# Optimization experiments

Hardware: AMD Instinct MI355X
Metric: run time of the kernel (lower is better)

## Reference

```python
import jax, jax.numpy as jnp
import numpy as np

B, N, D = 2, 2048, 1024
H, DH = 16, 64
INNER = H * DH  # 1024
EPS = 1e-5


def setup_inputs() -> dict:
    key = jax.random.key(0)
    ks = jax.random.split(key, 7)
    x = jax.random.normal(ks[0], (B, N, D), dtype=jnp.float32)
    mask = jax.random.uniform(ks[1], (B, N)) < 0.9
    mask = mask.at[:, 0].set(True)  # guarantee at least one valid key per row
    attn_bias = jax.random.normal(ks[2], (H, N, N), dtype=jnp.float32) * 0.02
    ln_w = jnp.ones((D,), dtype=jnp.float32)
    ln_b = jnp.zeros((D,), dtype=jnp.float32)
    wq = jax.random.normal(ks[3], (D, INNER), dtype=jnp.float32) * 0.02
    wkv = jax.random.normal(ks[4], (D, 2 * DH), dtype=jnp.float32) * 0.02
    wo = jax.random.normal(ks[5], (INNER, D), dtype=jnp.float32) * 0.02
    return {"x": x, "attn_bias": attn_bias, "ln_w": ln_w, "ln_b": ln_b,
            "wq": wq, "wkv": wkv, "wo": wo, "mask": mask}


def reference(x, attn_bias, ln_w, ln_b, wq, wkv, wo, mask):
    scale = DH ** -0.5
    # NOTE: in the torch module, kv_input = x BEFORE self.norm (context=None),
    # so K/V come from raw x while Q comes from LayerNorm(x).
    mu = jnp.mean(x, axis=-1, keepdims=True)
    var = jnp.var(x, axis=-1, keepdims=True)
    xn = (x - mu) / jnp.sqrt(var + EPS) * ln_w + ln_b
    q = (xn @ wq).reshape(B, N, H, DH).transpose(0, 2, 1, 3) * scale  # b h n d
    kv = x @ wkv                     # b n 2*dh (shared single KV head, MQA)
    k, v = kv[..., :DH], kv[..., DH:]
    sim = jnp.einsum('bhid,bjd->bhij', q, k) + attn_bias  # bias broadcasts over b
    mask_value = -jnp.finfo(sim.dtype).max
    sim = jnp.where(mask[:, None, None, :], sim, mask_value)
    attn = jax.nn.softmax(sim, axis=-1)
    out = jnp.einsum('bhij,bjd->bhid', attn, v)
    out = out.transpose(0, 2, 1, 3).reshape(B, N, INNER)
    return out @ wo
```

## Files before the change

### kernel.cpp

```cpp
#include <hip/hip_runtime.h>
#include <hip/hip_bf16.h>

typedef __bf16 bf16_t;
typedef __bf16 bf16x4 __attribute__((ext_vector_type(4)));
typedef __bf16 bf16x8 __attribute__((ext_vector_type(8)));
typedef float f32x4 __attribute__((ext_vector_type(4)));

static constexpr int BB    = 2;
static constexpr int SEQ   = 2048;
static constexpr int DM    = 1024;
static constexpr int NHEAD = 16;
static constexpr int HD    = 64;
static constexpr float L2E = 1.4426950408889634f;

__device__ __forceinline__ bf16x8 ld8(const bf16_t* p) {
  return *reinterpret_cast<const bf16x8*>(p);
}

__device__ __forceinline__ void gl_lds16(const bf16_t* g, bf16_t* l) {
  __builtin_amdgcn_global_load_lds(
      (const __attribute__((address_space(1))) void*)g,
      (__attribute__((address_space(3))) void*)l, 16, 0, 0);
}

__device__ __forceinline__ uint2 shfl2(uint2 v, int src) {
  uint2 r;
  r.x = (unsigned)__shfl((int)v.x, src, 64);
  r.y = (unsigned)__shfl((int)v.y, src, 64);
  return r;
}

template <typename T> __device__ __forceinline__ T cvt_out(float v);
template <> __device__ __forceinline__ float  cvt_out<float >(float v) { return v; }
template <> __device__ __forceinline__ bf16_t cvt_out<bf16_t>(float v) { return (bf16_t)v; }

__global__ __launch_bounds__(256) void transpose_cast(const float* __restrict__ in,
                                                      bf16_t* __restrict__ out,
                                                      int R, int C) {
  __shared__ float tile[32][33];
  const int c0 = blockIdx.x * 32, r0 = blockIdx.y * 32;
  const int tx = threadIdx.x & 31, ty = threadIdx.x >> 5;
#pragma unroll
  for (int y = ty; y < 32; y += 8)
    tile[y][tx] = in[(size_t)(r0 + y) * C + (c0 + tx)];
  __syncthreads();
#pragma unroll
  for (int y = ty; y < 32; y += 8)
    out[(size_t)(c0 + y) * R + (r0 + tx)] = (bf16_t)tile[tx][y];
}

__global__ __launch_bounds__(256) void row_prep(const float* __restrict__ x,
    const float* __restrict__ ln_w, const float* __restrict__ ln_b,
    const int* __restrict__ mask,
    bf16_t* __restrict__ xbf, bf16_t* __restrict__ xn, float* __restrict__ maskA) {
  const int row = blockIdx.x, t = threadIdx.x;
  __shared__ float red[8];
  const float4 xv = *reinterpret_cast<const float4*>(&x[(size_t)row * DM + t * 4]);
  float s  = xv.x + xv.y + xv.z + xv.w;
  float s2 = xv.x * xv.x + xv.y * xv.y + xv.z * xv.z + xv.w * xv.w;
#pragma unroll
  for (int off = 32; off >= 1; off >>= 1) {
    s  += __shfl_xor(s,  off, 64);
    s2 += __shfl_xor(s2, off, 64);
  }
  if ((t & 63) == 0) { red[t >> 6] = s; red[4 + (t >> 6)] = s2; }
  __syncthreads();
  s  = red[0] + red[1] + red[2] + red[3];
  s2 = red[4] + red[5] + red[6] + red[7];
  const float mu   = s * (1.0f / DM);
  const float var  = s2 * (1.0f / DM) - mu * mu;
  const float rstd = rsqrtf(var + 1e-5f);
  const float4 wv = *reinterpret_cast<const float4*>(&ln_w[t * 4]);
  const float4 bv = *reinterpret_cast<const float4*>(&ln_b[t * 4]);
  union { bf16_t h[4]; uint2 u; } p0, p1;
  p0.h[0] = (bf16_t)xv.x; p0.h[1] = (bf16_t)xv.y;
  p0.h[2] = (bf16_t)xv.z; p0.h[3] = (bf16_t)xv.w;
  p1.h[0] = (bf16_t)((xv.x - mu) * rstd * wv.x + bv.x);
  p1.h[1] = (bf16_t)((xv.y - mu) * rstd * wv.y + bv.y);
  p1.h[2] = (bf16_t)((xv.z - mu) * rstd * wv.z + bv.z);
  p1.h[3] = (bf16_t)((xv.w - mu) * rstd * wv.w + bv.w);
  *reinterpret_cast<uint2*>(&xbf[(size_t)row * DM + t * 4]) = p0.u;
  *reinterpret_cast<uint2*>(&xn [(size_t)row * DM + t * 4]) = p1.u;
  if (t == 0) maskA[row] = mask[row] ? 0.0f : -1e30f;
}

template <typename OutT>
__global__ __launch_bounds__(256) void gemm128(const bf16_t* __restrict__ A,
    const bf16_t* __restrict__ Bt, OutT* __restrict__ C,
    int M, int Nn, int K, float scale) {
  __shared__ alignas(16) bf16_t As[128 * 32];
  __shared__ alignas(16) bf16_t Bs[128 * 32];
  const int m0 = blockIdx.x * 128, n0 = blockIdx.y * 128;
  const int t = threadIdx.x, lane = t & 63, w = t >> 6;
  const int wm = (w & 1) * 64, wn = (w >> 1) * 64;
  const int l15 = lane & 15, q4 = lane >> 4;
  f32x4 acc[4][4] = {};
  const int sr = lane >> 2, sc = (lane & 3) * 8;
  const bf16_t* Ap0 = A  + (size_t)(m0 + w * 32 + sr) * K + sc;
  const bf16_t* Ap1 = Ap0 + (size_t)16 * K;
  const bf16_t* Bp0 = Bt + (size_t)(n0 + w * 32 + sr) * K + sc;
  const bf16_t* Bp1 = Bp0 + (size_t)16 * K;
  bf16_t* AsL0 = &As[(w * 32) * 32];
  bf16_t* AsL1 = &As[(w * 32 + 16) * 32];
  bf16_t* BsL0 = &Bs[(w * 32) * 32];
  bf16_t* BsL1 = &Bs[(w * 32 + 16) * 32];
  for (int k0 = 0; k0 < K; k0 += 32) {
    gl_lds16(Ap0 + k0, AsL0);
    gl_lds16(Ap1 + k0, AsL1);
    gl_lds16(Bp0 + k0, BsL0);
    gl_lds16(Bp1 + k0, BsL1);
    __syncthreads();
    bf16x8 af[4], bfr[4];
#pragma unroll
    for (int mt = 0; mt < 4; ++mt) af[mt]  = ld8(&As[(wm + mt * 16 + l15) * 32 + q4 * 8]);
#pragma unroll
    for (int nt = 0; nt < 4; ++nt) bfr[nt] = ld8(&Bs[(wn + nt * 16 + l15) * 32 + q4 * 8]);
#pragma unroll
    for (int mt = 0; mt < 4; ++mt)
#pragma unroll
      for (int nt = 0; nt < 4; ++nt)
        acc[mt][nt] = __builtin_amdgcn_mfma_f32_16x16x32_bf16(af[mt], bfr[nt], acc[mt][nt], 0, 0, 0);
    __syncthreads();
  }
#pragma unroll
  for (int mt = 0; mt < 4; ++mt)
#pragma unroll
    for (int nt = 0; nt < 4; ++nt)
#pragma unroll
      for (int r = 0; r < 4; ++r) {
        const int gm = m0 + wm + mt * 16 + q4 * 4 + r;
        const int gn = n0 + wn + nt * 16 + l15;
        C[(size_t)gm * Nn + gn] = cvt_out<OutT>(acc[mt][nt][r] * scale);
      }
}

__global__ __launch_bounds__(256) void gemm_kv(const bf16_t* __restrict__ A,
    const bf16_t* __restrict__ Bt, bf16_t* __restrict__ C, bf16_t* __restrict__ C2,
    int M, int Nn, int K) {
  __shared__ alignas(16) bf16_t As[128 * 32];
  __shared__ alignas(16) bf16_t Bs[64 * 32];
  const int m0 = blockIdx.x * 128, n0 = blockIdx.y * 64;
  const int t = threadIdx.x, lane = t & 63, w = t >> 6;
  const int wm = (w & 1) * 64, wn = (w >> 1) * 32;
  const int l15 = lane & 15, q4 = lane >> 4;
  f32x4 acc[4][2] = {};
  const int sr = lane >> 2, sc = (lane & 3) * 8;
  const bf16_t* Ap0 = A  + (size_t)(m0 + w * 32 + sr) * K + sc;
  const bf16_t* Ap1 = Ap0 + (size_t)16 * K;
  const bf16_t* Bp  = Bt + (size_t)(n0 + w * 16 + sr) * K + sc;
  bf16_t* AsL0 = &As[(w * 32) * 32];
  bf16_t* AsL1 = &As[(w * 32 + 16) * 32];
  bf16_t* BsL  = &Bs[(w * 16) * 32];
  for (int k0 = 0; k0 < K; k0 += 32) {
    gl_lds16(Ap0 + k0, AsL0);
    gl_lds16(Ap1 + k0, AsL1);
    gl_lds16(Bp  + k0, BsL);
    __syncthreads();
    bf16x8 af[4], bfr[2];
#pragma unroll
    for (int mt = 0; mt < 4; ++mt) af[mt]  = ld8(&As[(wm + mt * 16 + l15) * 32 + q4 * 8]);
#pragma unroll
    for (int nt = 0; nt < 2; ++nt) bfr[nt] = ld8(&Bs[(wn + nt * 16 + l15) * 32 + q4 * 8]);
#pragma unroll
    for (int mt = 0; mt < 4; ++mt)
#pragma unroll
      for (int nt = 0; nt < 2; ++nt)
        acc[mt][nt] = __builtin_amdgcn_mfma_f32_16x16x32_bf16(af[mt], bfr[nt], acc[mt][nt], 0, 0, 0);
    __syncthreads();
  }
#pragma unroll
  for (int mt = 0; mt < 4; ++mt)
#pragma unroll
    for (int nt = 0; nt < 2; ++nt)
#pragma unroll
      for (int r = 0; r < 4; ++r) {
        const int gm = m0 + wm + mt * 16 + q4 * 4 + r;
        const int gn = n0 + wn + nt * 16 + l15;
        const bf16_t ov = (bf16_t)acc[mt][nt][r];
        if (gn < HD) C[(size_t)gm * HD + gn] = ov;
        else C2[((size_t)(gm >> 11) * HD + (gn - HD)) * SEQ + (gm & 2047)] = ov;
      }
}

__global__ __launch_bounds__(256, 4) void flash_attn(
    const bf16_t* __restrict__ q,
    const bf16_t* __restrict__ kk,
    const bf16_t* __restrict__ vT,
    const float*  __restrict__ bias,
    const float*  __restrict__ maskA,
    bf16_t* __restrict__ aout)
{
  const int b = blockIdx.y & 1, h = blockIdx.y >> 1;
  const int i0 = blockIdx.x * 64;
  const int t = threadIdx.x, lane = t & 63, w = t >> 6;
  const int l15 = lane & 15, q4 = lane >> 4;

  __shared__ alignas(16) bf16_t Ks[2][64][72];
  __shared__ alignas(16) bf16_t Vs[2][64][72];

  const bf16_t* qrow = &q[((size_t)b * SEQ + i0 + w * 16 + l15) * DM + h * HD];
  const bf16x8 bq0 = ld8(qrow + q4 * 8);
  const bf16x8 bq1 = ld8(qrow + 32 + q4 * 8);

  f32x4 o[4] = {};
  float m_run = -1e30f, l_run = 0.0f;

  const float* bias_p = bias + (size_t)h * SEQ * SEQ
                      + (size_t)(i0 + w * 16 + l15) * SEQ + q4 * 4;
  const float* mask_p = maskA + b * SEQ + q4 * 4;

  const int sr = t >> 2, sc = (t & 3) * 16;
  const bf16_t* kp = &kk[((size_t)b * SEQ + sr) * HD + sc];
  const bf16_t* vp = &vT[((size_t)b * HD + sr) * SEQ + sc];

  uint4 kr0 = *reinterpret_cast<const uint4*>(kp);
  uint4 kr1 = *reinterpret_cast<const uint4*>(kp + 8);
  uint4 vr0 = *reinterpret_cast<const uint4*>(vp);
  uint4 vr1 = *reinterpret_cast<const uint4*>(vp + 8);
  f32x4 bv[4], mv[4];
#pragma unroll
  for (int mt = 0; mt < 4; ++mt) {
    bv[mt] = *reinterpret_cast<const f32x4*>(bias_p + mt * 16);
    mv[mt] = *reinterpret_cast<const f32x4*>(mask_p + mt * 16);
  }
  *reinterpret_cast<uint4*>(&Ks[0][sr][sc])     = kr0;
  *reinterpret_cast<uint4*>(&Ks[0][sr][sc + 8]) = kr1;
  *reinterpret_cast<uint4*>(&Vs[0][sr][sc])     = vr0;
  *reinterpret_cast<uint4*>(&Vs[0][sr][sc + 8]) = vr1;
  __syncthreads();

  for (int it = 0; it < SEQ / 64; ++it) {
    const int buf = it & 1;
    const int j1 = (it + 1) * 64;
    const bool more = (j1 < SEQ);
    if (more) {
      kr0 = *reinterpret_cast<const uint4*>(kp + (size_t)j1 * HD);
      kr1 = *reinterpret_cast<const uint4*>(kp + (size_t)j1 * HD + 8);
      vr0 = *reinterpret_cast<const uint4*>(vp + j1);
      vr1 = *reinterpret_cast<const uint4*>(vp + j1 + 8);
    }

    f32x4 s[4];
#pragma unroll
    for (int mt = 0; mt < 4; ++mt) {
      const bf16x8 a0 = ld8(&Ks[buf][mt * 16 + l15][q4 * 8]);
      const bf16x8 a1 = ld8(&Ks[buf][mt * 16 + l15][32 + q4 * 8]);
      f32x4 z = {0.f, 0.f, 0.f, 0.f};
      z = __builtin_amdgcn_mfma_f32_16x16x32_bf16(a0, bq0, z, 0, 0, 0);
      z = __builtin_amdgcn_mfma_f32_16x16x32_bf16(a1, bq1, z, 0, 0, 0);
      s[mt] = z;
    }

    float mx = -1e30f;
#pragma unroll
    for (int mt = 0; mt < 4; ++mt)
#pragma unroll
      for (int r = 0; r < 4; ++r) {
        s[mt][r] = s[mt][r] + bv[mt][r] + mv[mt][r];
        mx = fmaxf(mx, s[mt][r]);
      }
    if (more) {
#pragma unroll
      for (int mt = 0; mt < 4; ++mt) {
        bv[mt] = *reinterpret_cast<const f32x4*>(bias_p + j1 + mt * 16);
        mv[mt] = *reinterpret_cast<const f32x4*>(mask_p + j1 + mt * 16);
      }
    }
    mx = fmaxf(mx, __shfl_xor(mx, 16, 64));
    mx = fmaxf(mx, __shfl_xor(mx, 32, 64));
    const float mnew  = fmaxf(m_run, mx);
    const float alpha = __builtin_amdgcn_exp2f((m_run - mnew) * L2E);
    const float cc    = -mnew * L2E;
    m_run = mnew;

    float su = 0.0f;
#pragma unroll
    for (int mt = 0; mt < 4; ++mt)
#pragma unroll
      for (int r = 0; r < 4; ++r) {
        s[mt][r] = __builtin_amdgcn_exp2f(__builtin_fmaf(s[mt][r], L2E, cc));
        su += s[mt][r];
      }
    su += __shfl_xor(su, 16, 64);
    su += __shfl_xor(su, 32, 64);
    l_run = l_run * alpha + su;

#pragma unroll
    for (int r = 0; r < 4; ++r) {
      const float a_r = __shfl(alpha, q4 * 4 + r, 64);
      o[0][r] *= a_r; o[1][r] *= a_r; o[2][r] *= a_r; o[3][r] *= a_r;
    }

    uint2 pk[4];
#pragma unroll
    for (int mt = 0; mt < 4; ++mt) {
      union { bf16_t hh[4]; uint2 u; } pu;
      pu.hh[0] = (bf16_t)s[mt][0]; pu.hh[1] = (bf16_t)s[mt][1];
      pu.hh[2] = (bf16_t)s[mt][2]; pu.hh[3] = (bf16_t)s[mt][3];
      pk[mt] = pu.u;
    }
    const int src0 = ((q4 & 1) << 5) + l15;
    const int src1 = src0 + 16;
    const bool hiSel = (q4 >> 1) != 0;
#pragma unroll
    for (int ks = 0; ks < 2; ++ks) {
      const uint2 a0 = shfl2(pk[2 * ks],     src0);
      const uint2 a1 = shfl2(pk[2 * ks + 1], src0);
      const uint2 b0 = shfl2(pk[2 * ks],     src1);
      const uint2 b1 = shfl2(pk[2 * ks + 1], src1);
      union { unsigned u[4]; bf16x8 v; } pf;
      pf.u[0] = hiSel ? a1.x : a0.x; pf.u[1] = hiSel ? a1.y : a0.y;
      pf.u[2] = hiSel ? b1.x : b0.x; pf.u[3] = hiSel ? b1.y : b0.y;
#pragma unroll
      for (int nt = 0; nt < 4; ++nt) {
        const bf16x8 vv = ld8(&Vs[buf][nt * 16 + l15][ks * 32 + q4 * 8]);
        o[nt] = __builtin_amdgcn_mfma_f32_16x16x32_bf16(pf.v, vv, o[nt], 0, 0, 0);
      }
    }

    if (more) {
      *reinterpret_cast<uint4*>(&Ks[buf ^ 1][sr][sc])     = kr0;
      *reinterpret_cast<uint4*>(&Ks[buf ^ 1][sr][sc + 8]) = kr1;
      *reinterpret_cast<uint4*>(&Vs[buf ^ 1][sr][sc])     = vr0;
      *reinterpret_cast<uint4*>(&Vs[buf ^ 1][sr][sc + 8]) = vr1;
    }
    __syncthreads();
  }

#pragma unroll
  for (int r = 0; r < 4; ++r) {
    const float linv = 1.0f / __shfl(l_run, q4 * 4 + r, 64);
    const int gi = i0 + w * 16 + q4 * 4 + r;
    bf16_t* dst = &aout[((size_t)b * SEQ + gi) * DM + h * HD];
#pragma unroll
    for (int nt = 0; nt < 4; ++nt)
      dst[nt * 16 + l15] = (bf16_t)(o[nt][r] * linv);
  }
}

extern "C" void kernel_launch(void* const* d_in, const int* in_sizes, int n_in,
                              void* d_out, int out_size, void* d_ws, size_t ws_size,
                              hipStream_t stream) {
  const float* x         = (const float*)d_in[0];
  const float* attn_bias = (const float*)d_in[1];
  const float* ln_w      = (const float*)d_in[2];
  const float* ln_b      = (const float*)d_in[3];
  const float* wq        = (const float*)d_in[4];
  const float* wkv       = (const float*)d_in[5];
  const float* wo        = (const float*)d_in[6];
  const int*   mask      = (const int*)d_in[7];
  float* out = (float*)d_out;

  char* ws = (char*)d_ws;
  size_t off = 0;
  auto alloc = [&](size_t bytes) {
    char* p = ws + off;
    off += (bytes + 255) & ~(size_t)255;
    return p;
  };
  bf16_t* xbf   = (bf16_t*)alloc((size_t)BB * SEQ * DM * 2);
  bf16_t* xn    = (bf16_t*)alloc((size_t)BB * SEQ * DM * 2);
  bf16_t* wqT   = (bf16_t*)alloc((size_t)DM * DM * 2);
  bf16_t* wkvT  = (bf16_t*)alloc((size_t)2 * HD * DM * 2);
  bf16_t* woT   = (bf16_t*)alloc((size_t)DM * DM * 2);
  bf16_t* qb    = (bf16_t*)alloc((size_t)BB * SEQ * DM * 2);
  bf16_t* kkb   = (bf16_t*)alloc((size_t)BB * SEQ * HD * 2);
  bf16_t* vTb   = (bf16_t*)alloc((size_t)BB * HD * SEQ * 2);
  bf16_t* aoutb = (bf16_t*)alloc((size_t)BB * SEQ * DM * 2);
  float*  maskA = (float*)alloc((size_t)BB * SEQ * 4);

  transpose_cast<<<dim3(DM / 32, DM / 32), 256, 0, stream>>>(wq, wqT, DM, DM);
  transpose_cast<<<dim3(128 / 32, DM / 32), 256, 0, stream>>>(wkv, wkvT, DM, 128);
  transpose_cast<<<dim3(DM / 32, DM / 32), 256, 0, stream>>>(wo, woT, DM, DM);
  row_prep<<<BB * SEQ, 256, 0, stream>>>(x, ln_w, ln_b, mask, xbf, xn, maskA);
  gemm128<bf16_t><<<dim3(32, 8), 256, 0, stream>>>(xn, wqT, qb, BB * SEQ, DM, DM, 0.125f);
  gemm_kv<<<dim3(32, 2), 256, 0, stream>>>(xbf, wkvT, kkb, vTb, BB * SEQ, 128, DM);
  flash_attn<<<dim3(SEQ / 64, BB * NHEAD), 256, 0, stream>>>(qb, kkb, vTb, attn_bias,
                                                             maskA, aoutb);
  gemm128<float><<<dim3(32, 8), 256, 0, stream>>>(aoutb, woT, out, BB * SEQ, DM, DM, 1.0f);
}
```

Measured before the change: 512.9 us.

## Double-buffer GEMM LDS loads, fuse Q and KV GEMMs, prioritize attention MFMAs

```diff
diff --git a/kernel.cpp b/kernel.cpp
--- a/kernel.cpp
+++ b/kernel.cpp
@@ -84,44 +84,68 @@
   if (t == 0) maskA[row] = mask[row] ? 0.0f : -1e30f;
 }
 
-template <typename OutT>
-__global__ __launch_bounds__(256) void gemm128(const bf16_t* __restrict__ A,
-    const bf16_t* __restrict__ Bt, OutT* __restrict__ C,
-    int M, int Nn, int K, float scale) {
-  __shared__ alignas(16) bf16_t As[128 * 32];
-  __shared__ alignas(16) bf16_t Bs[128 * 32];
-  const int m0 = blockIdx.x * 128, n0 = blockIdx.y * 128;
+__device__ __forceinline__ void gemm_core_db(
+    const bf16_t* __restrict__ A, const bf16_t* __restrict__ Bt, int K,
+    int m0, int n0, bf16_t* As, bf16_t* Bs, f32x4 (&acc)[4][4]) {
   const int t = threadIdx.x, lane = t & 63, w = t >> 6;
   const int wm = (w & 1) * 64, wn = (w >> 1) * 64;
   const int l15 = lane & 15, q4 = lane >> 4;
-  f32x4 acc[4][4] = {};
   const int sr = lane >> 2, sc = (lane & 3) * 8;
   const bf16_t* Ap0 = A  + (size_t)(m0 + w * 32 + sr) * K + sc;
   const bf16_t* Ap1 = Ap0 + (size_t)16 * K;
   const bf16_t* Bp0 = Bt + (size_t)(n0 + w * 32 + sr) * K + sc;
   const bf16_t* Bp1 = Bp0 + (size_t)16 * K;
-  bf16_t* AsL0 = &As[(w * 32) * 32];
-  bf16_t* AsL1 = &As[(w * 32 + 16) * 32];
-  bf16_t* BsL0 = &Bs[(w * 32) * 32];
-  bf16_t* BsL1 = &Bs[(w * 32 + 16) * 32];
+  const int la0 = (w * 32) * 32, la1 = (w * 32 + 16) * 32;
+  gl_lds16(Ap0, As + la0);
+  gl_lds16(Ap1, As + la1);
+  gl_lds16(Bp0, Bs + la0);
+  gl_lds16(Bp1, Bs + la1);
+  __syncthreads();
+  int buf = 0;
   for (int k0 = 0; k0 < K; k0 += 32) {
-    gl_lds16(Ap0 + k0, AsL0);
-    gl_lds16(Ap1 + k0, AsL1);
-    gl_lds16(Bp0 + k0, BsL0);
-    gl_lds16(Bp1 + k0, BsL1);
-    __syncthreads();
+    const int nbuf = buf ^ 1;
+    if (k0 + 32 < K) {
+      const int kn = k0 + 32;
+      gl_lds16(Ap0 + kn, As + nbuf * (128 * 32) + la0);
+      gl_lds16(Ap1 + kn, As + nbuf * (128 * 32) + la1);
+      gl_lds16(Bp0 + kn, Bs + nbuf * (128 * 32) + la0);
+      gl_lds16(Bp1 + kn, Bs + nbuf * (128 * 32) + la1);
+    }
+    const bf16_t* Asb = As + buf * (128 * 32);
+    const bf16_t* Bsb = Bs + buf * (128 * 32);
     bf16x8 af[4], bfr[4];
 #pragma unroll
-    for (int mt = 0; mt < 4; ++mt) af[mt]  = ld8(&As[(wm + mt * 16 + l15) * 32 + q4 * 8]);
-#pragma unroll
-    for (int nt = 0; nt < 4; ++nt) bfr[nt] = ld8(&Bs[(wn + nt * 16 + l15) * 32 + q4 * 8]);
+    for (int mt = 0; mt < 4; ++mt) af[mt]  = ld8(&Asb[(wm + mt * 16 + l15) * 32 + q4 * 8]);
+#pragma unroll
+    for (int nt = 0; nt < 4; ++nt) bfr[nt] = ld8(&Bsb[(wn + nt * 16 + l15) * 32 + q4 * 8]);
 #pragma unroll
     for (int mt = 0; mt < 4; ++mt)
 #pragma unroll
       for (int nt = 0; nt < 4; ++nt)
         acc[mt][nt] = __builtin_amdgcn_mfma_f32_16x16x32_bf16(af[mt], bfr[nt], acc[mt][nt], 0, 0, 0);
     __syncthreads();
-  }
+    buf = nbuf;
+  }
+}
+
+__global__ __launch_bounds__(256) void gemm_qkv(
+    const bf16_t* __restrict__ xn,  const bf16_t* __restrict__ wqT,  bf16_t* __restrict__ qb,
+    const bf16_t* __restrict__ xbf, const bf16_t* __restrict__ wkvT,
+    bf16_t* __restrict__ kkb, bf16_t* __restrict__ vTb) {
+  __shared__ alignas(16) bf16_t As[2][128 * 32];
+  __shared__ alignas(16) bf16_t Bs[2][128 * 32];
+  const int bx = blockIdx.x;
+  const bool isKV = (bx < 32);
+  const int m0 = isKV ? bx * 128 : ((bx - 32) & 31) * 128;
+  const int n0 = isKV ? 0 : ((bx - 32) >> 5) * 128;
+  const bf16_t* A  = isKV ? xbf  : xn;
+  const bf16_t* Bt = isKV ? wkvT : wqT;
+  f32x4 acc[4][4] = {};
+  gemm_core_db(A, Bt, DM, m0, n0, &As[0][0], &Bs[0][0], acc);
+
+  const int lane = threadIdx.x & 63, w = threadIdx.x >> 6;
+  const int wm = (w & 1) * 64, wn = (w >> 1) * 64;
+  const int l15 = lane & 15, q4 = lane >> 4;
 #pragma unroll
   for (int mt = 0; mt < 4; ++mt)
 #pragma unroll
@@ -130,55 +154,35 @@
       for (int r = 0; r < 4; ++r) {
         const int gm = m0 + wm + mt * 16 + q4 * 4 + r;
         const int gn = n0 + wn + nt * 16 + l15;
-        C[(size_t)gm * Nn + gn] = cvt_out<OutT>(acc[mt][nt][r] * scale);
-      }
-}
-
-__global__ __launch_bounds__(256) void gemm_kv(const bf16_t* __restrict__ A,
-    const bf16_t* __restrict__ Bt, bf16_t* __restrict__ C, bf16_t* __restrict__ C2,
-    int M, int Nn, int K) {
-  __shared__ alignas(16) bf16_t As[128 * 32];
-  __shared__ alignas(16) bf16_t Bs[64 * 32];
-  const int m0 = blockIdx.x * 128, n0 = blockIdx.y * 64;
-  const int t = threadIdx.x, lane = t & 63, w = t >> 6;
-  const int wm = (w & 1) * 64, wn = (w >> 1) * 32;
+        if (isKV) {
+          const bf16_t ov = (bf16_t)acc[mt][nt][r];
+          if (gn < HD) kkb[(size_t)gm * HD + gn] = ov;
+          else vTb[((size_t)(gm >> 11) * HD + (gn - HD)) * SEQ + (gm & 2047)] = ov;
+        } else {
+          qb[(size_t)gm * DM + gn] = (bf16_t)(acc[mt][nt][r] * 0.125f);
+        }
+      }
+}
+
+__global__ __launch_bounds__(256) void gemm_out(const bf16_t* __restrict__ A,
+    const bf16_t* __restrict__ Bt, float* __restrict__ C, int K) {
+  __shared__ alignas(16) bf16_t As[2][128 * 32];
+  __shared__ alignas(16) bf16_t Bs[2][128 * 32];
+  const int m0 = blockIdx.x * 128, n0 = blockIdx.y * 128;
+  f32x4 acc[4][4] = {};
+  gemm_core_db(A, Bt, K, m0, n0, &As[0][0], &Bs[0][0], acc);
+  const int lane = threadIdx.x & 63, w = threadIdx.x >> 6;
+  const int wm = (w & 1) * 64, wn = (w >> 1) * 64;
   const int l15 = lane & 15, q4 = lane >> 4;
-  f32x4 acc[4][2] = {};
-  const int sr = lane >> 2, sc = (lane & 3) * 8;
-  const bf16_t* Ap0 = A  + (size_t)(m0 + w * 32 + sr) * K + sc;
-  const bf16_t* Ap1 = Ap0 + (size_t)16 * K;
-  const bf16_t* Bp  = Bt + (size_t)(n0 + w * 16 + sr) * K + sc;
-  bf16_t* AsL0 = &As[(w * 32) * 32];
-  bf16_t* AsL1 = &As[(w * 32 + 16) * 32];
-  bf16_t* BsL  = &Bs[(w * 16) * 32];
-  for (int k0 = 0; k0 < K; k0 += 32) {
-    gl_lds16(Ap0 + k0, AsL0);
-    gl_lds16(Ap1 + k0, AsL1);
-    gl_lds16(Bp  + k0, BsL);
-    __syncthreads();
-    bf16x8 af[4], bfr[2];
-#pragma unroll
-    for (int mt = 0; mt < 4; ++mt) af[mt]  = ld8(&As[(wm + mt * 16 + l15) * 32 + q4 * 8]);
-#pragma unroll
-    for (int nt = 0; nt < 2; ++nt) bfr[nt] = ld8(&Bs[(wn + nt * 16 + l15) * 32 + q4 * 8]);
-#pragma unroll
-    for (int mt = 0; mt < 4; ++mt)
-#pragma unroll
-      for (int nt = 0; nt < 2; ++nt)
-        acc[mt][nt] = __builtin_amdgcn_mfma_f32_16x16x32_bf16(af[mt], bfr[nt], acc[mt][nt], 0, 0, 0);
-    __syncthreads();
-  }
 #pragma unroll
   for (int mt = 0; mt < 4; ++mt)
 #pragma unroll
-    for (int nt = 0; nt < 2; ++nt)
+    for (int nt = 0; nt < 4; ++nt)
 #pragma unroll
       for (int r = 0; r < 4; ++r) {
         const int gm = m0 + wm + mt * 16 + q4 * 4 + r;
         const int gn = n0 + wn + nt * 16 + l15;
-        const bf16_t ov = (bf16_t)acc[mt][nt][r];
-        if (gn < HD) C[(size_t)gm * HD + gn] = ov;
-        else C2[((size_t)(gm >> 11) * HD + (gn - HD)) * SEQ + (gm & 2047)] = ov;
+        C[(size_t)gm * DM + gn] = acc[mt][nt][r];
       }
 }
 
@@ -217,11 +221,12 @@
   uint4 kr1 = *reinterpret_cast<const uint4*>(kp + 8);
   uint4 vr0 = *reinterpret_cast<const uint4*>(vp);
   uint4 vr1 = *reinterpret_cast<const uint4*>(vp + 8);
-  f32x4 bv[4], mv[4];
+  f32x4 bm[4];
 #pragma unroll
   for (int mt = 0; mt < 4; ++mt) {
-    bv[mt] = *reinterpret_cast<const f32x4*>(bias_p + mt * 16);
-    mv[mt] = *reinterpret_cast<const f32x4*>(mask_p + mt * 16);
+    const f32x4 bv = *reinterpret_cast<const f32x4*>(bias_p + mt * 16);
+    const f32x4 mv = *reinterpret_cast<const f32x4*>(mask_p + mt * 16);
+    bm[mt] = bv + mv;
   }
   *reinterpret_cast<uint4*>(&Ks[0][sr][sc])     = kr0;
   *reinterpret_cast<uint4*>(&Ks[0][sr][sc + 8]) = kr1;
@@ -241,6 +246,7 @@
     }
 
     f32x4 s[4];
+    __builtin_amdgcn_s_setprio(1);
 #pragma unroll
     for (int mt = 0; mt < 4; ++mt) {
       const bf16x8 a0 = ld8(&Ks[buf][mt * 16 + l15][q4 * 8]);
@@ -250,20 +256,22 @@
       z = __builtin_amdgcn_mfma_f32_16x16x32_bf16(a1, bq1, z, 0, 0, 0);
       s[mt] = z;
     }
+    __builtin_amdgcn_s_setprio(0);
 
     float mx = -1e30f;
 #pragma unroll
     for (int mt = 0; mt < 4; ++mt)
 #pragma unroll
       for (int r = 0; r < 4; ++r) {
-        s[mt][r] = s[mt][r] + bv[mt][r] + mv[mt][r];
+        s[mt][r] = s[mt][r] + bm[mt][r];
         mx = fmaxf(mx, s[mt][r]);
       }
     if (more) {
 #pragma unroll
       for (int mt = 0; mt < 4; ++mt) {
-        bv[mt] = *reinterpret_cast<const f32x4*>(bias_p + j1 + mt * 16);
-        mv[mt] = *reinterpret_cast<const f32x4*>(mask_p + j1 + mt * 16);
+        const f32x4 bv = *reinterpret_cast<const f32x4*>(bias_p + j1 + mt * 16);
+        const f32x4 mv = *reinterpret_cast<const f32x4*>(mask_p + j1 + mt * 16);
+        bm[mt] = bv + mv;
       }
     }
     mx = fmaxf(mx, __shfl_xor(mx, 16, 64));
@@ -311,11 +319,13 @@
       union { unsigned u[4]; bf16x8 v; } pf;
       pf.u[0] = hiSel ? a1.x : a0.x; pf.u[1] = hiSel ? a1.y : a0.y;
       pf.u[2] = hiSel ? b1.x : b0.x; pf.u[3] = hiSel ? b1.y : b0.y;
+      __builtin_amdgcn_s_setprio(1);
 #pragma unroll
       for (int nt = 0; nt < 4; ++nt) {
         const bf16x8 vv = ld8(&Vs[buf][nt * 16 + l15][ks * 32 + q4 * 8]);
         o[nt] = __builtin_amdgcn_mfma_f32_16x16x32_bf16(pf.v, vv, o[nt], 0, 0, 0);
       }
+      __builtin_amdgcn_s_setprio(0);
     }
 
     if (more) {
@@ -373,9 +383,8 @@
   transpose_cast<<<dim3(128 / 32, DM / 32), 256, 0, stream>>>(wkv, wkvT, DM, 128);
   transpose_cast<<<dim3(DM / 32, DM / 32), 256, 0, stream>>>(wo, woT, DM, DM);
   row_prep<<<BB * SEQ, 256, 0, stream>>>(x, ln_w, ln_b, mask, xbf, xn, maskA);
-  gemm128<bf16_t><<<dim3(32, 8), 256, 0, stream>>>(xn, wqT, qb, BB * SEQ, DM, DM, 0.125f);
-  gemm_kv<<<dim3(32, 2), 256, 0, stream>>>(xbf, wkvT, kkb, vTb, BB * SEQ, 128, DM);
+  gemm_qkv<<<288, 256, 0, stream>>>(xn, wqT, qb, xbf, wkvT, kkb, vTb);
   flash_attn<<<dim3(SEQ / 64, BB * NHEAD), 256, 0, stream>>>(qb, kkb, vTb, attn_bias,
                                                              maskA, aoutb);
-  gemm128<float><<<dim3(32, 8), 256, 0, stream>>>(aoutb, woT, out, BB * SEQ, DM, DM, 1.0f);
-}
+  gemm_out<<<dim3(32, 8), 256, 0, stream>>>(aoutb, woT, out, DM);
+}
```

After: 527.6 us. 1.03x slower.
